# Kernel tuning notes

Measured on AMD Instinct MI355X. Metric: run time of the kernel, lower is better.

## Reference

```python
import jax, jax.numpy as jnp
import numpy as np

N = 500_000          # minibatch nodes
NUM_NODES = 1_000_000  # embedding table rows
F0 = 500_000         # raw feature table rows for ntype 0
DIN = 256            # raw feature dim for ntype 0
D = 128              # embed_size


def setup_inputs() -> dict:
    key = jax.random.key(0)
    k0, k1, k2, k3, k4, k5 = jax.random.split(key, 6)
    feat0 = jax.random.normal(k0, (F0, DIN), dtype=jnp.float32)
    # xavier-uniform-ish scale for the projection
    lim = float(np.sqrt(6.0 / (DIN + D)))
    W0 = jax.random.uniform(k1, (DIN, D), dtype=jnp.float32, minval=-lim, maxval=lim)
    # node_embeds initialized uniform(-1, 1)
    emb_table = jax.random.uniform(k2, (NUM_NODES, D), dtype=jnp.float32, minval=-1.0, maxval=1.0)
    node_ids = jax.random.randint(k3, (N,), 0, NUM_NODES, dtype=jnp.int32)
    node_tids = jax.random.randint(k4, (N,), 0, 2, dtype=jnp.int32)
    type_ids = jax.random.randint(k5, (N,), 0, F0, dtype=jnp.int32)
    return {"feat0": feat0, "W0": W0, "emb_table": emb_table,
            "node_ids": node_ids, "node_tids": node_tids, "type_ids": type_ids}


def reference(feat0, W0, emb_table, node_ids, node_tids, type_ids):
    # Original loops over node types, building per-type blocks and an index
    # map idx so that the final embeds[idx] restores the original node order.
    # That is equivalent to, per node i:
    #   out[i] = feat0[type_ids[i]] @ W0   if node_tids[i] == 0 (featured type)
    #   out[i] = emb_table[node_ids[i]]    if node_tids[i] == 1 (featureless)
    proj = feat0[type_ids] @ W0          # [N, D] gather + tall-skinny matmul
    emb = emb_table[node_ids]            # [N, D] embedding lookup
    is_featured = (node_tids == 0)[:, None]
    return jnp.where(is_featured, proj, emb)
```

## Files before the change

### kernel.cpp

```cpp
#include <hip/hip_runtime.h>
#include <hip/hip_bf16.h>

#define DIN 256
#define DOUT 128

using short8  = __attribute__((ext_vector_type(8))) short;
using floatx4 = __attribute__((ext_vector_type(4))) float;

__device__ __forceinline__ unsigned short f2bf(float f) {
    union { float f; unsigned u; } x; x.f = f;
    unsigned u = x.u;
    unsigned r = u + 0x7fffu + ((u >> 16) & 1u);
    return (unsigned short)(r >> 16);
}

__global__ void w0_pack_kernel(const float* __restrict__ W0,
                               unsigned short* __restrict__ Bfrag) {
    int e = blockIdx.x * blockDim.x + threadIdx.x;
    int j  = e & 7;
    int l  = (e >> 3) & 63;
    int ks = (e >> 9) & 7;
    int ct = e >> 12;
    int k = ks * 32 + (l >> 4) * 8 + j;
    int c = ct * 16 + (l & 15);
    Bfrag[e] = f2bf(W0[k * DOUT + c]);
}

__global__ __launch_bounds__(512, 2) void fused_embed_kernel(
    const float* __restrict__ feat0,
    const float* __restrict__ emb_table,
    const unsigned short* __restrict__ Bfrag,
    const int* __restrict__ node_ids,
    const int* __restrict__ node_tids,
    const int* __restrict__ type_ids,
    float* __restrict__ out,
    int n)
{
    __shared__ short8 sB[4096];

    const int t  = threadIdx.x;
    const int w  = t >> 6;
    const int l  = t & 63;
    const int lr = l & 15;
    const int kg = l >> 4;

    {
        const short8* src = reinterpret_cast<const short8*>(Bfrag);
        short8 tmp[8];
        #pragma unroll
        for (int j = 0; j < 8; ++j) tmp[j] = src[t + j * 512];
        #pragma unroll
        for (int j = 0; j < 8; ++j) sB[t + j * 512] = tmp[j];
    }

    const long long nodebase = (long long)blockIdx.x * 128 + w * 16;
    const long long myrow = nodebase + lr;
    int tid = 1, gt = 0, gn = 0;
    if (myrow < n) {
        tid = node_tids[myrow];
        gt  = type_ids[myrow];
        gn  = node_ids[myrow];
    }

    __syncthreads();

    const bool featured = (tid == 0);
    const int  gts = featured ? gt : 0;
    const float4* arow = reinterpret_cast<const float4*>(
        feat0 + (long long)gts * DIN) + kg * 2;
    float4 av[16];
    #pragma unroll
    for (int ks = 0; ks < 8; ++ks) {
        av[2 * ks]     = arow[ks * 8];
        av[2 * ks + 1] = arow[ks * 8 + 1];
    }

    const int crow = l >> 2;
    const int csub = l & 3;
    const int t_c  = __shfl(tid, crow);
    const int gn_c = __shfl(gn, crow);
    const long long cnode = nodebase + crow;
    const bool copyrow = (t_c == 1) && (cnode < n);
    const int  gns = copyrow ? gn_c : 0;
    const float4* esrc = reinterpret_cast<const float4*>(
        emb_table + (long long)gns * DOUT);
    float4 ev[8];
    #pragma unroll
    for (int j = 0; j < 8; ++j) ev[j] = esrc[csub + j * 4];

    floatx4 acc[8];
    #pragma unroll
    for (int ct = 0; ct < 8; ++ct) acc[ct] = (floatx4){0.f, 0.f, 0.f, 0.f};
    #pragma unroll
    for (int ks = 0; ks < 8; ++ks) {
        const float4 a0 = av[2 * ks];
        const float4 a1 = av[2 * ks + 1];
        short8 af;
        af[0] = (short)f2bf(a0.x); af[1] = (short)f2bf(a0.y);
        af[2] = (short)f2bf(a0.z); af[3] = (short)f2bf(a0.w);
        af[4] = (short)f2bf(a1.x); af[5] = (short)f2bf(a1.y);
        af[6] = (short)f2bf(a1.z); af[7] = (short)f2bf(a1.w);
        #pragma unroll
        for (int ct = 0; ct < 8; ++ct)
            acc[ct] = __builtin_amdgcn_mfma_f32_16x16x32_bf16(
                af, sB[(ct * 8 + ks) * 64 + l], acc[ct], 0, 0, 0);
    }

    #pragma unroll
    for (int r = 0; r < 4; ++r) {
        const int row = kg * 4 + r;
        const int t_r = __shfl(tid, row);
        const long long node = nodebase + row;
        if (t_r == 0 && node < n) {
            float* orow = out + node * DOUT;
            #pragma unroll
            for (int ct = 0; ct < 8; ++ct)
                orow[ct * 16 + lr] = acc[ct][r];
        }
    }

    if (copyrow) {
        float4* dst = reinterpret_cast<float4*>(out + cnode * DOUT);
        #pragma unroll
        for (int j = 0; j < 8; ++j) dst[csub + j * 4] = ev[j];
    }
}

extern "C" void kernel_launch(void* const* d_in, const int* in_sizes, int n_in,
                              void* d_out, int out_size, void* d_ws, size_t ws_size,
                              hipStream_t stream) {
    const float* feat0      = (const float*)d_in[0];
    const float* W0         = (const float*)d_in[1];
    const float* emb_table  = (const float*)d_in[2];
    const int*   node_ids   = (const int*)d_in[3];
    const int*   node_tids  = (const int*)d_in[4];
    const int*   type_ids   = (const int*)d_in[5];
    float*       out        = (float*)d_out;
    const int n = in_sizes[3];

    unsigned short* Bfrag = (unsigned short*)d_ws;

    hipLaunchKernelGGL(w0_pack_kernel, dim3((DIN * DOUT) / 256), dim3(256),
                       0, stream, W0, Bfrag);

    const int grid = (n + 127) / 128;
    hipLaunchKernelGGL(fused_embed_kernel, dim3(grid), dim3(512), 0, stream,
                       feat0, emb_table, Bfrag, node_ids, node_tids, type_ids,
                       out, n);
}
```

Measured before the change: 154.4 us.

## Make waves persistent over multiple tiles with software-pipelined gathers

Each wave now processes T=8 consecutive 16-node tiles instead of one. While the current tile is converted and multiplied, it prefetches the next tile's feature and embedding rows and the indices two tiles ahead. This cuts the per-block cost of loading W0 into LDS (8x fewer blocks) and overlaps gather latency with MFMA work. In exchange it raises register pressure (double-held A fragments and prefetch buffers) and leaves far fewer blocks (~490), which may hurt latency hiding through occupancy.

```diff
diff --git a/kernel.cpp b/kernel.cpp
--- a/kernel.cpp
+++ b/kernel.cpp
@@ -34,15 +34,17 @@
     const int* __restrict__ node_tids,
     const int* __restrict__ type_ids,
     float* __restrict__ out,
-    int n)
+    int n, int T)
 {
     __shared__ short8 sB[4096];
 
-    const int t  = threadIdx.x;
-    const int w  = t >> 6;
-    const int l  = t & 63;
-    const int lr = l & 15;
-    const int kg = l >> 4;
+    const int t    = threadIdx.x;
+    const int w    = t >> 6;
+    const int l    = t & 63;
+    const int lr   = l & 15;
+    const int kg   = l >> 4;
+    const int crow = l >> 2;
+    const int csub = l & 3;
 
     {
         const short8* src = reinterpret_cast<const short8*>(Bfrag);
@@ -53,76 +55,107 @@
         for (int j = 0; j < 8; ++j) sB[t + j * 512] = tmp[j];
     }
 
-    const long long nodebase = (long long)blockIdx.x * 128 + w * 16;
-    const long long myrow = nodebase + lr;
-    int tid = 1, gt = 0, gn = 0;
-    if (myrow < n) {
-        tid = node_tids[myrow];
-        gt  = type_ids[myrow];
-        gn  = node_ids[myrow];
-    }
+    const long long wbase = ((long long)blockIdx.x * 8 + w) * ((long long)T * 16);
+
+    float4 av[16];
+    float4 ev[8];
+
+    auto loadIdx = [&](int tt, int& tid, int& gt, int& gn) {
+        tid = -1; gt = 0; gn = 0;
+        if (tt < T) {
+            const long long row = wbase + (long long)tt * 16 + lr;
+            if (row < n) { tid = node_tids[row]; gt = type_ids[row]; gn = node_ids[row]; }
+        }
+    };
+    auto issueA = [&](int tid, int gt) {
+        const int gts = (tid == 0) ? gt : 0;
+        const float4* arow = reinterpret_cast<const float4*>(
+            feat0 + (long long)gts * DIN) + kg * 2;
+        #pragma unroll
+        for (int ks = 0; ks < 8; ++ks) {
+            av[2 * ks]     = arow[ks * 8];
+            av[2 * ks + 1] = arow[ks * 8 + 1];
+        }
+    };
+    auto issueE = [&](int tid, int gn_self) {
+        const int t_c  = __shfl(tid, crow);
+        const int gn_c = __shfl(gn_self, crow);
+        const int gns  = (t_c == 1) ? gn_c : 0;
+        const float4* esrc = reinterpret_cast<const float4*>(
+            emb_table + (long long)gns * DOUT);
+        #pragma unroll
+        for (int j = 0; j < 8; ++j) ev[j] = esrc[csub + j * 4];
+    };
+
+    int tidC, gtC, gnC, tidN, gtN, gnN;
+    loadIdx(0, tidC, gtC, gnC);
+    loadIdx(1, tidN, gtN, gnN);
+    issueA(tidC, gtC);
+    issueE(tidC, gnC);
 
     __syncthreads();
 
-    const bool featured = (tid == 0);
-    const int  gts = featured ? gt : 0;
-    const float4* arow = reinterpret_cast<const float4*>(
-        feat0 + (long long)gts * DIN) + kg * 2;
-    float4 av[16];
-    #pragma unroll
-    for (int ks = 0; ks < 8; ++ks) {
-        av[2 * ks]     = arow[ks * 8];
-        av[2 * ks + 1] = arow[ks * 8 + 1];
-    }
+    for (int tt = 0; tt < T; ++tt) {
+        const long long nodebase = wbase + (long long)tt * 16;
+        const int tidS = tidC;
 
-    const int crow = l >> 2;
-    const int csub = l & 3;
-    const int t_c  = __shfl(tid, crow);
-    const int gn_c = __shfl(gn, crow);
-    const long long cnode = nodebase + crow;
-    const bool copyrow = (t_c == 1) && (cnode < n);
-    const int  gns = copyrow ? gn_c : 0;
-    const float4* esrc = reinterpret_cast<const float4*>(
-        emb_table + (long long)gns * DOUT);
-    float4 ev[8];
-    #pragma unroll
-    for (int j = 0; j < 8; ++j) ev[j] = esrc[csub + j * 4];
+        short8 afs[8];
+        #pragma unroll
+        for (int ks = 0; ks < 8; ++ks) {
+            const float4 a0 = av[2 * ks];
+            const float4 a1 = av[2 * ks + 1];
+            short8 af;
+            af[0] = (short)f2bf(a0.x); af[1] = (short)f2bf(a0.y);
+            af[2] = (short)f2bf(a0.z); af[3] = (short)f2bf(a0.w);
+            af[4] = (short)f2bf(a1.x); af[5] = (short)f2bf(a1.y);
+            af[6] = (short)f2bf(a1.z); af[7] = (short)f2bf(a1.w);
+            afs[ks] = af;
+        }
 
-    floatx4 acc[8];
-    #pragma unroll
-    for (int ct = 0; ct < 8; ++ct) acc[ct] = (floatx4){0.f, 0.f, 0.f, 0.f};
-    #pragma unroll
-    for (int ks = 0; ks < 8; ++ks) {
-        const float4 a0 = av[2 * ks];
-        const float4 a1 = av[2 * ks + 1];
-        short8 af;
-        af[0] = (short)f2bf(a0.x); af[1] = (short)f2bf(a0.y);
-        af[2] = (short)f2bf(a0.z); af[3] = (short)f2bf(a0.w);
-        af[4] = (short)f2bf(a1.x); af[5] = (short)f2bf(a1.y);
-        af[6] = (short)f2bf(a1.z); af[7] = (short)f2bf(a1.w);
+        {
+            const int t_c = __shfl(tidS, crow);
+            const long long cnode = nodebase + crow;
+            if (t_c == 1 && cnode < n) {
+                float4* dst = reinterpret_cast<float4*>(out + cnode * DOUT);
+                #pragma unroll
+                for (int j = 0; j < 8; ++j) dst[csub + j * 4] = ev[j];
+            }
+        }
+
+        if (tt + 1 < T) {
+            issueA(tidN, gtN);
+            issueE(tidN, gnN);
+        }
+
+        int tid2, gt2, gn2;
+        loadIdx(tt + 2, tid2, gt2, gn2);
+
+        floatx4 acc[8];
         #pragma unroll
-        for (int ct = 0; ct < 8; ++ct)
-            acc[ct] = __builtin_amdgcn_mfma_f32_16x16x32_bf16(
-                af, sB[(ct * 8 + ks) * 64 + l], acc[ct], 0, 0, 0);
-    }
-
-    #pragma unroll
-    for (int r = 0; r < 4; ++r) {
-        const int row = kg * 4 + r;
-        const int t_r = __shfl(tid, row);
-        const long long node = nodebase + row;
-        if (t_r == 0 && node < n) {
-            float* orow = out + node * DOUT;
+        for (int ct = 0; ct < 8; ++ct) acc[ct] = (floatx4){0.f, 0.f, 0.f, 0.f};
+        #pragma unroll
+        for (int ks = 0; ks < 8; ++ks) {
             #pragma unroll
             for (int ct = 0; ct < 8; ++ct)
-                orow[ct * 16 + lr] = acc[ct][r];
+                acc[ct] = __builtin_amdgcn_mfma_f32_16x16x32_bf16(
+                    afs[ks], sB[(ct * 8 + ks) * 64 + l], acc[ct], 0, 0, 0);
         }
-    }
 
-    if (copyrow) {
-        float4* dst = reinterpret_cast<float4*>(out + cnode * DOUT);
         #pragma unroll
-        for (int j = 0; j < 8; ++j) dst[csub + j * 4] = ev[j];
+        for (int r = 0; r < 4; ++r) {
+            const int row = kg * 4 + r;
+            const int t_r = __shfl(tidS, row);
+            const long long node = nodebase + row;
+            if (t_r == 0 && node < n) {
+                float* orow = out + node * DOUT;
+                #pragma unroll
+                for (int ct = 0; ct < 8; ++ct)
+                    orow[ct * 16 + lr] = acc[ct][r];
+            }
+        }
+
+        tidC = tidN; gtC = gtN; gnC = gnN;
+        tidN = tid2; gtN = gt2; gnN = gn2;
     }
 }
 
@@ -143,8 +176,10 @@
     hipLaunchKernelGGL(w0_pack_kernel, dim3((DIN * DOUT) / 256), dim3(256),
                        0, stream, W0, Bfrag);
 
-    const int grid = (n + 127) / 128;
+    const int T = 8;
+    const int wtiles = (n + 15) / 16;
+    const int grid = (wtiles + 8 * T - 1) / (8 * T);
     hipLaunchKernelGGL(fused_embed_kernel, dim3(grid), dim3(512), 0, stream,
                        feat0, emb_table, Bfrag, node_ids, node_tids, type_ids,
-                       out, n);
+                       out, n, T);
 }
```

Measured after the change: 549.1 us. 3.56x slower.
